# Optimization experiments

Measured on AMD Instinct MI355X. Metric: run time of the kernel, lower is better.

## Reference

```python
import jax, jax.numpy as jnp
import numpy as np

EPS = 1e-5  # torch InstanceNorm2d default eps

def conv1x1(x, w, b):
    # x: [B,C,H,W], w: [O,C], b: [O]
    return jnp.einsum('bchw,oc->bohw', x, w) + b[None, :, None, None]

def instance_norm(x):
    # InstanceNorm2d(affine=False): normalize per-sample, per-channel over H,W
    mean = jnp.mean(x, axis=(2, 3), keepdims=True)
    var = jnp.var(x, axis=(2, 3), keepdims=True)
    return (x - mean) * jax.lax.rsqrt(var + EPS)

def proj(x, w, b):
    return jax.nn.relu(instance_norm(conv1x1(x, w, b)))

def setup_inputs() -> dict:
    key = jax.random.key(0)
    ks = jax.random.split(key, 9)
    B, C, Ci, H, W = 16, 256, 128, 64, 64
    s_in = 1.0 / np.sqrt(C)
    s_mid = 1.0 / np.sqrt(Ci)
    return {
        'x': jax.random.normal(ks[0], (B, C, H, W), jnp.float32),
        'g_w': jax.random.normal(ks[1], (Ci, C), jnp.float32) * s_in,
        'g_b': jax.random.normal(ks[2], (Ci,), jnp.float32) * s_in,
        'theta_w': jax.random.normal(ks[3], (Ci, C), jnp.float32) * s_in,
        'theta_b': jax.random.normal(ks[4], (Ci,), jnp.float32) * s_in,
        'phi_w': jax.random.normal(ks[5], (Ci, C), jnp.float32) * s_in,
        'phi_b': jax.random.normal(ks[6], (Ci,), jnp.float32) * s_in,
        'W_w': jax.random.normal(ks[7], (C, Ci), jnp.float32) * s_mid,
        'W_b': jax.random.normal(ks[8], (C,), jnp.float32) * s_mid,
    }

def reference(x, g_w, g_b, theta_w, theta_b, phi_w, phi_b, W_w, W_b):
    B, C, H, W = x.shape
    Ci = g_w.shape[0]
    N = H * W
    g_x = proj(x, g_w, g_b).reshape(B, Ci, N)        # [B,Ci,N]
    theta_x = proj(x, theta_w, theta_b).reshape(B, Ci, N)
    phi_x = proj(x, phi_w, phi_b).reshape(B, Ci, N)
    # channel-attention Gram matrix [B,Ci,Ci], softmax over last dim
    f = jnp.einsum('bin,bjn->bij', theta_x, phi_x)
    attn = jax.nn.softmax(f, axis=2)
    y = jnp.einsum('bij,bjn->bin', attn, g_x)        # [B,Ci,N]
    # replicate torch permute(0,2,1).contiguous().view(B,Ci,H,W)
    y = jnp.transpose(y, (0, 2, 1)).reshape(B, Ci, H, W)
    y = instance_norm(conv1x1(y, W_w, W_b))
    return y + x
```

## Files before the change

kernel.cpp:

```cpp
#include <hip/hip_runtime.h>

#define DEVINL __device__ __forceinline__

typedef __attribute__((ext_vector_type(8))) short bf8v;
typedef __attribute__((ext_vector_type(4))) float f32x4;
typedef __attribute__((ext_vector_type(8))) unsigned short us8;
typedef __attribute__((ext_vector_type(4))) unsigned short us4;

DEVINL unsigned short f2bf(float f) {
  unsigned int u = __builtin_bit_cast(unsigned int, f);
  u += 0x7fffu + ((u >> 16) & 1u);
  return (unsigned short)(u >> 16);
}
DEVINL unsigned short f2bf_trunc(float f) {
  return (unsigned short)(__builtin_bit_cast(unsigned int, f) >> 16);
}
DEVINL float bf2f(unsigned short h) {
  unsigned int u = ((unsigned int)h) << 16;
  return __builtin_bit_cast(float, u);
}

__global__ __launch_bounds__(512, 4)
void proj_gemm(const unsigned short* __restrict__ wall_hi,
               const unsigned short* __restrict__ wall_lo,
               const float* __restrict__ x,
               unsigned short* __restrict__ zr_hi, unsigned short* __restrict__ zr_lo,
               float* __restrict__ partials)
{
  __shared__ __align__(16) unsigned short As_hi[384 * 40];
  __shared__ __align__(16) unsigned short As_lo[256 * 40];
  __shared__ __align__(16) unsigned short Bs_hi[64 * 40];
  __shared__ __align__(16) unsigned short Bs_lo[64 * 40];

  const int t = threadIdx.x;
  const int lane = t & 63;
  const int wave = t >> 6;
  const int wm = wave >> 1, wn = wave & 1;
  const int lr = lane & 15, lk = lane >> 4;
  const int b = blockIdx.z;
  const int bx = blockIdx.x;
  const int nbase = bx * 64;
  const float* xs = x + (long)b * 256 * 4096;

  f32x4 acc[6][2];
#pragma unroll
  for (int i = 0; i < 6; ++i)
#pragma unroll
    for (int j = 0; j < 2; ++j) acc[i][j] = (f32x4)0.0f;

  for (int kt = 0; kt < 8; ++kt) {
    const int k0 = kt * 32;
#pragma unroll
    for (int i = 0; i < 3; ++i) {
      const int q = i * 512 + t;
      const int row = q >> 2, c = q & 3;
      *(us8*)&As_hi[row * 40 + c * 8] = *(const us8*)&wall_hi[(long)row * 256 + k0 + c * 8];
    }
#pragma unroll
    for (int i = 0; i < 2; ++i) {
      const int q = i * 512 + t;
      const int row = q >> 2, c = q & 3;
      *(us8*)&As_lo[row * 40 + c * 8] = *(const us8*)&wall_lo[(long)row * 256 + k0 + c * 8];
    }
    const int nl = t & 63, cg = t >> 6;
    float xv[4];
#pragma unroll
    for (int i = 0; i < 4; ++i)
      xv[i] = xs[(long)(k0 + cg * 4 + i) * 4096 + nbase + nl];
    us4 h4, l4;
#pragma unroll
    for (int e = 0; e < 4; ++e) {
      const float v = xv[e];
      const unsigned short hb = f2bf(v);
      h4[e] = hb;
      l4[e] = f2bf_trunc(v - bf2f(hb));
    }
    *(us4*)&Bs_hi[nl * 40 + cg * 4] = h4;
    *(us4*)&Bs_lo[nl * 40 + cg * 4] = l4;
    __syncthreads();

    const int ko = lk * 8;
    bf8v bh[2], bl[2];
#pragma unroll
    for (int ni = 0; ni < 2; ++ni) {
      const int r = (wn * 32 + ni * 16 + lr) * 40 + ko;
      bh[ni] = *(const bf8v*)&Bs_hi[r];
      bl[ni] = *(const bf8v*)&Bs_lo[r];
    }
#pragma unroll
    for (int mi = 0; mi < 6; ++mi) {
      const int fr = mi * 4 + wm;
      const int r = (fr * 16 + lr) * 40 + ko;
      const bf8v ah = *(const bf8v*)&As_hi[r];
      if (fr < 16) {
        const bf8v al = *(const bf8v*)&As_lo[r];
#pragma unroll
        for (int ni = 0; ni < 2; ++ni) {
          acc[mi][ni] = __builtin_amdgcn_mfma_f32_16x16x32_bf16(bh[ni], ah, acc[mi][ni], 0, 0, 0);
          acc[mi][ni] = __builtin_amdgcn_mfma_f32_16x16x32_bf16(bl[ni], ah, acc[mi][ni], 0, 0, 0);
          acc[mi][ni] = __builtin_amdgcn_mfma_f32_16x16x32_bf16(bh[ni], al, acc[mi][ni], 0, 0, 0);
        }
      } else {
#pragma unroll
        for (int ni = 0; ni < 2; ++ni)
          acc[mi][ni] = __builtin_amdgcn_mfma_f32_16x16x32_bf16(bh[ni], ah, acc[mi][ni], 0, 0, 0);
      }
    }
    __syncthreads();
  }

  float* sbuf = (float*)As_hi;
#pragma unroll
  for (int mi = 0; mi < 6; ++mi) {
    float s = 0.f, ss = 0.f;
#pragma unroll
    for (int ni = 0; ni < 2; ++ni)
#pragma unroll
      for (int r = 0; r < 4; ++r) {
        const float v = acc[mi][ni][r];
        s += v; ss += v * v;
      }
    const int fr = mi * 4 + wm;
    const int slot = ((fr * 16 + lr) * 8 + (wn * 4 + lk)) * 2;
    sbuf[slot] = s; sbuf[slot + 1] = ss;
  }
  __syncthreads();
  if (t < 384) {
    float s = 0.f, ss = 0.f;
#pragma unroll
    for (int w = 0; w < 8; ++w) {
      s += sbuf[(t * 8 + w) * 2];
      ss += sbuf[(t * 8 + w) * 2 + 1];
    }
    const long pidx = ((long)bx * 6144 + b * 384 + t) * 2;
    partials[pidx] = s; partials[pidx + 1] = ss;
  }

#pragma unroll
  for (int mi = 0; mi < 6; ++mi)
#pragma unroll
    for (int ni = 0; ni < 2; ++ni) {
      const int gm = (mi * 4 + wm) * 16 + lr;
      const int gn = nbase + wn * 32 + ni * 16 + lk * 4;
      const long o = ((long)b * 384 + gm) * 4096 + gn;
      us4 hv, lv;
#pragma unroll
      for (int r = 0; r < 4; ++r) {
        const float v = acc[mi][ni][r];
        const unsigned short h = f2bf(v);
        hv[r] = h;
        lv[r] = f2bf_trunc(v - bf2f(h));
      }
      *(us4*)&zr_hi[o] = hv;
      *(us4*)&zr_lo[o] = lv;
    }
}

__global__ __launch_bounds__(256)
void stats_reduce(const float* __restrict__ partials, float* __restrict__ stats)
{
  const int row = blockIdx.x * 256 + threadIdx.x;
  float s = 0.f, ss = 0.f;
#pragma unroll
  for (int k = 0; k < 64; ++k) {
    s += partials[((long)k * 6144 + row) * 2];
    ss += partials[((long)k * 6144 + row) * 2 + 1];
  }
  const float mean = s * (1.f / 4096.f);
  const float var = ss * (1.f / 4096.f) - mean * mean;
  const float rs = rsqrtf(fmaxf(var, 0.f) + 1e-5f);
  stats[row * 2] = rs;
  stats[row * 2 + 1] = -mean * rs;
}

__global__ __launch_bounds__(256, 4)
void fgemm_norm(const unsigned short* __restrict__ zr_hi, const unsigned short* __restrict__ zr_lo,
                const float* __restrict__ stats, float* __restrict__ fpart)
{
  __shared__ __align__(16) unsigned short As_hi[128 * 72];
  __shared__ __align__(16) unsigned short As_lo[128 * 72];
  __shared__ __align__(16) unsigned short Bs_hi[128 * 72];
  __shared__ __align__(16) unsigned short Bs_lo[128 * 72];

  const int t = threadIdx.x;
  const int lane = t & 63;
  const int wave = t >> 6;
  const int wm = wave >> 1, wn = wave & 1;
  const int lr = lane & 15, lk = lane >> 4;
  const int zb = blockIdx.z >> 5, z1 = blockIdx.z & 31;
  const int koff = z1 * 128;

  f32x4 acc[4][4];
#pragma unroll
  for (int i = 0; i < 4; ++i)
#pragma unroll
    for (int j = 0; j < 4; ++j) acc[i][j] = (f32x4)0.0f;

  for (int kt = 0; kt < 2; ++kt) {
    const int k0 = koff + kt * 64;
#pragma unroll
    for (int i = 0; i < 4; ++i) {
      const int q = i * 256 + t;
      const int row = q >> 3, c = q & 7;
#pragma unroll
      for (int op = 0; op < 2; ++op) {
        const int grow = zb * 384 + op * 128 + row;
        const long g = (long)grow * 4096 + k0 + c * 8;
        const us8 h = *(const us8*)&zr_hi[g];
        const us8 l = *(const us8*)&zr_lo[g];
        const float rs = stats[grow * 2];
        const float nmrs = stats[grow * 2 + 1];
        us8 oh, ol;
#pragma unroll
        for (int e = 0; e < 8; ++e) {
          const float v = bf2f(h[e]) + bf2f(l[e]);
          const float nv = fmaxf(__builtin_fmaf(v, rs, nmrs), 0.f);
          const unsigned short hb = f2bf(nv);
          oh[e] = hb;
          ol[e] = f2bf_trunc(nv - bf2f(hb));
        }
        unsigned short* dh = op ? Bs_hi : As_hi;
        unsigned short* dl = op ? Bs_lo : As_lo;
        *(us8*)&dh[row * 72 + c * 8] = oh;
        *(us8*)&dl[row * 72 + c * 8] = ol;
      }
    }
    __syncthreads();
#pragma unroll
    for (int ks = 0; ks < 2; ++ks) {
      const int ko = ks * 32 + lk * 8;
      bf8v ah[4], bh[4], al[4], bl[4];
#pragma unroll
      for (int mi = 0; mi < 4; ++mi) {
        const int r = (wm * 64 + mi * 16 + lr) * 72 + ko;
        ah[mi] = *(const bf8v*)&As_hi[r];
        al[mi] = *(const bf8v*)&As_lo[r];
      }
#pragma unroll
      for (int ni = 0; ni < 4; ++ni) {
        const int r = (wn * 64 + ni * 16 + lr) * 72 + ko;
        bh[ni] = *(const bf8v*)&Bs_hi[r];
        bl[ni] = *(const bf8v*)&Bs_lo[r];
      }
#pragma unroll
      for (int mi = 0; mi < 4; ++mi)
#pragma unroll
        for (int ni = 0; ni < 4; ++ni) {
          acc[mi][ni] = __builtin_amdgcn_mfma_f32_16x16x32_bf16(bh[ni], ah[mi], acc[mi][ni], 0, 0, 0);
          acc[mi][ni] = __builtin_amdgcn_mfma_f32_16x16x32_bf16(bl[ni], ah[mi], acc[mi][ni], 0, 0, 0);
          acc[mi][ni] = __builtin_amdgcn_mfma_f32_16x16x32_bf16(bh[ni], al[mi], acc[mi][ni], 0, 0, 0);
        }
    }
    __syncthreads();
  }

  const long cOff = ((long)zb * 32 + z1) * 16384;
#pragma unroll
  for (int mi = 0; mi < 4; ++mi)
#pragma unroll
    for (int ni = 0; ni < 4; ++ni) {
      const int gm = wm * 64 + mi * 16 + lr;
      const int gn = wn * 64 + ni * 16 + lk * 4;
      *(f32x4*)&fpart[cOff + (long)gm * 128 + gn] = acc[mi][ni];
    }
}

template<bool OUT_BF16>
__global__ __launch_bounds__(256, 2)
void gemm_tn(const unsigned short* __restrict__ Ah0, const unsigned short* __restrict__ Bh0,
             void* __restrict__ Cout,
             int lda, int ldb, int ldc, int ksteps, int z1count,
             long aS1, long aS2, long bS1, long bS2, long cS1, long cS2)
{
  __shared__ __align__(16) unsigned short As_hi[128 * 72];
  __shared__ __align__(16) unsigned short Bs_hi[128 * 72];

  const int t = threadIdx.x;
  const int lane = t & 63;
  const int wave = t >> 6;
  const int wm = wave >> 1, wn = wave & 1;
  const int lr = lane & 15, lk = lane >> 4;

  const int z = blockIdx.z;
  const int zb = z / z1count, z1 = z - zb * z1count;
  const unsigned short* Ah = Ah0 + zb * aS2 + z1 * aS1;
  const unsigned short* Bh = Bh0 + zb * bS2 + z1 * bS1;
  const long cOff = zb * cS2 + z1 * cS1;

  const int mbase = blockIdx.y * 128;
  const int nbase = blockIdx.x * 128;

  f32x4 acc[4][4];
#pragma unroll
  for (int i = 0; i < 4; ++i)
#pragma unroll
    for (int j = 0; j < 4; ++j) acc[i][j] = (f32x4)0.0f;

  for (int kt = 0; kt < ksteps; ++kt) {
    const int k0 = kt * 64;
#pragma unroll
    for (int i = 0; i < 4; ++i) {
      const int q = i * 256 + t;
      const int row = q >> 3, c = q & 7;
      const int lo = row * 72 + c * 8;
      *(us8*)&As_hi[lo] = *(const us8*)&Ah[(long)(mbase + row) * lda + k0 + c * 8];
      *(us8*)&Bs_hi[lo] = *(const us8*)&Bh[(long)(nbase + row) * ldb + k0 + c * 8];
    }
    __syncthreads();
#pragma unroll
    for (int ks = 0; ks < 2; ++ks) {
      const int ko = ks * 32 + lk * 8;
      bf8v ah[4], bh[4];
#pragma unroll
      for (int mi = 0; mi < 4; ++mi)
        ah[mi] = *(const bf8v*)&As_hi[(wm * 64 + mi * 16 + lr) * 72 + ko];
#pragma unroll
      for (int ni = 0; ni < 4; ++ni)
        bh[ni] = *(const bf8v*)&Bs_hi[(wn * 64 + ni * 16 + lr) * 72 + ko];
#pragma unroll
      for (int mi = 0; mi < 4; ++mi)
#pragma unroll
        for (int ni = 0; ni < 4; ++ni)
          acc[mi][ni] = __builtin_amdgcn_mfma_f32_16x16x32_bf16(bh[ni], ah[mi], acc[mi][ni], 0, 0, 0);
    }
    __syncthreads();
  }

#pragma unroll
  for (int mi = 0; mi < 4; ++mi)
#pragma unroll
    for (int ni = 0; ni < 4; ++ni) {
      const int gm = mbase + wm * 64 + mi * 16 + lr;
      const int gn = nbase + wn * 64 + ni * 16 + lk * 4;
      const f32x4 v = acc[mi][ni];
      if (OUT_BF16) {
        us4 o;
#pragma unroll
        for (int r = 0; r < 4; ++r) o[r] = f2bf(v[r]);
        *(us4*)&((unsigned short*)Cout)[cOff + (long)gm * ldc + gn] = o;
      } else {
        *(f32x4*)&((float*)Cout)[cOff + (long)gm * ldc + gn] = v;
      }
    }
}

__global__ __launch_bounds__(256)
void prep_weights(const float* __restrict__ g_w, const float* __restrict__ th_w,
                  const float* __restrict__ ph_w, const float* __restrict__ W_w,
                  unsigned short* __restrict__ wall_hi, unsigned short* __restrict__ wall_lo,
                  unsigned short* __restrict__ w2h)
{
  const int i = blockIdx.x * 256 + threadIdx.x;
  float v;
  if (i < 32768) v = th_w[i];
  else if (i < 65536) v = ph_w[i - 32768];
  else v = g_w[i - 65536];
  const unsigned short h = f2bf(v);
  wall_hi[i] = h;
  if (i < 65536) wall_lo[i] = f2bf_trunc(v - bf2f(h));
  if (i < 32768) w2h[i] = f2bf(W_w[i]);
}

__global__ __launch_bounds__(256)
void norm_transpose_g(const unsigned short* __restrict__ zr_hi,
                      const unsigned short* __restrict__ zr_lo,
                      const float* __restrict__ stats,
                      unsigned short* __restrict__ gT)
{
  __shared__ unsigned short T[64 * 136];
  const int b = blockIdx.y, n0 = blockIdx.x * 64;
  const int t = threadIdx.x;
  const int c = t >> 1, part = t & 1;
  const int grow = b * 384 + 256 + c;
  const float rs = stats[grow * 2];
  const float nmrs = stats[grow * 2 + 1];
  const long off = (long)grow * 4096 + n0 + part * 32;
#pragma unroll
  for (int j = 0; j < 8; ++j) {
    const us4 h = *(const us4*)&zr_hi[off + j * 4];
    const us4 l = *(const us4*)&zr_lo[off + j * 4];
#pragma unroll
    for (int e = 0; e < 4; ++e) {
      const float v = bf2f(h[e]) + bf2f(l[e]);
      const float nv = fmaxf(__builtin_fmaf(v, rs, nmrs), 0.f);
      T[(part * 32 + j * 4 + e) * 136 + c] = f2bf(nv);
    }
  }
  __syncthreads();
  const int nl = t >> 2, q = t & 3;
  const long obase = ((long)b * 4096 + n0 + nl) * 128 + q * 32;
#pragma unroll
  for (int k = 0; k < 4; ++k) {
    us8 o;
#pragma unroll
    for (int e = 0; e < 8; ++e) o[e] = T[nl * 136 + q * 32 + k * 8 + e];
    *(us8*)&gT[obase + k * 8] = o;
  }
}

__global__ __launch_bounds__(64)
void softmax_attn(const float* __restrict__ fpart, unsigned short* __restrict__ attn)
{
  const int row = blockIdx.x;
  const int b = row >> 7, i = row & 127;
  const int t = threadIdx.x;
  float v0 = 0.f, v1 = 0.f;
#pragma unroll
  for (int kc = 0; kc < 32; ++kc) {
    const float* p = fpart + ((long)(b * 32 + kc)) * 16384 + i * 128;
    v0 += p[t];
    v1 += p[t + 64];
  }
  float mx = fmaxf(v0, v1);
  for (int o = 32; o > 0; o >>= 1) mx = fmaxf(mx, __shfl_xor(mx, o));
  const float e0 = __expf(v0 - mx), e1 = __expf(v1 - mx);
  float s = e0 + e1;
  for (int o = 32; o > 0; o >>= 1) s += __shfl_xor(s, o);
  const float inv = 1.f / s;
  attn[(long)row * 128 + t] = f2bf(e0 * inv);
  attn[(long)row * 128 + t + 64] = f2bf(e1 * inv);
}

__global__ __launch_bounds__(256)
void finalize(const unsigned short* __restrict__ z2b, const float* __restrict__ x,
              float* __restrict__ out)
{
  const int row = blockIdx.x;
  const long base = (long)row * 4096;
  const int t = threadIdx.x;
  float v[16];
  float s = 0.f, ss = 0.f;
#pragma unroll
  for (int h = 0; h < 2; ++h) {
    us8 u = *(const us8*)&z2b[base + t * 16 + h * 8];
#pragma unroll
    for (int e = 0; e < 8; ++e) {
      const float f = bf2f(u[e]);
      v[h * 8 + e] = f;
      s += f; ss += f * f;
    }
  }
  __shared__ float r0[256], r1[256];
  r0[t] = s; r1[t] = ss;
  __syncthreads();
  for (int o = 128; o > 0; o >>= 1) {
    if (t < o) { r0[t] += r0[t + o]; r1[t] += r1[t + o]; }
    __syncthreads();
  }
  const float mean = r0[0] * (1.f / 4096.f);
  const float var = r1[0] * (1.f / 4096.f) - mean * mean;
  const float rs = rsqrtf(fmaxf(var, 0.f) + 1e-5f);
#pragma unroll
  for (int i = 0; i < 4; ++i) {
    f32x4 xr = *(const f32x4*)&x[base + t * 16 + i * 4];
    f32x4 o;
#pragma unroll
    for (int e = 0; e < 4; ++e) o[e] = (v[i * 4 + e] - mean) * rs + xr[e];
    *(f32x4*)&out[base + t * 16 + i * 4] = o;
  }
}

extern "C" void kernel_launch(void* const* d_in, const int* in_sizes, int n_in,
                              void* d_out, int out_size, void* d_ws, size_t ws_size,
                              hipStream_t stream)
{
  const float* x    = (const float*)d_in[0];
  const float* g_w  = (const float*)d_in[1];
  const float* th_w = (const float*)d_in[3];
  const float* ph_w = (const float*)d_in[5];
  const float* W_w  = (const float*)d_in[7];

  char* ws = (char*)d_ws;
  const size_t MB = 1024ull * 1024ull;
  if (ws_size < 186 * MB) return;

  unsigned short* zr_hi    = (unsigned short*)(ws);
  unsigned short* zr_lo    = (unsigned short*)(ws + 48 * MB);
  float*          fpart    = (float*)(ws + 96 * MB);
  unsigned short* attn     = (unsigned short*)(ws + 128 * MB);
  unsigned short* gT       = (unsigned short*)(ws + 132 * MB);
  unsigned short* y4T      = (unsigned short*)(ws + 148 * MB);
  unsigned short* z2b      = (unsigned short*)(ws);
  float*          partials = (float*)(ws + 164 * MB);
  float*          stats    = (float*)(ws + 167 * MB);
  unsigned short* wall_hi  = (unsigned short*)(ws + 168 * MB);
  unsigned short* wall_lo  = (unsigned short*)(ws + 168 * MB + 256 * 1024);
  unsigned short* w2h      = (unsigned short*)(ws + 168 * MB + 512 * 1024);

  prep_weights<<<dim3(384), 256, 0, stream>>>(g_w, th_w, ph_w, W_w, wall_hi, wall_lo, w2h);

  proj_gemm<<<dim3(64, 1, 16), 512, 0, stream>>>(wall_hi, wall_lo, x, zr_hi, zr_lo, partials);

  stats_reduce<<<dim3(24), 256, 0, stream>>>(partials, stats);

  norm_transpose_g<<<dim3(64, 16), 256, 0, stream>>>(zr_hi, zr_lo, stats, gT);

  fgemm_norm<<<dim3(1, 1, 512), 256, 0, stream>>>(zr_hi, zr_lo, stats, fpart);

  softmax_attn<<<dim3(2048), 64, 0, stream>>>(fpart, attn);

  gemm_tn<true><<<dim3(1, 1, 512), 256, 0, stream>>>(
      attn, gT, y4T,
      128, 4096, 128, 2, 32,
      0, 16384, 128, (long)4096 * 128, 16384, (long)4096 * 128);

  gemm_tn<true><<<dim3(32, 2, 16), 256, 0, stream>>>(
      w2h, y4T, z2b,
      128, 128, 4096, 2, 1,
      0, 0, 0, (long)4096 * 128, 0, (long)256 * 4096);

  finalize<<<dim3(4096), 256, 0, stream>>>(z2b, x, (float*)d_out);
}
```

Before: 174.4 us.

## Enlarge proj GEMM tile with register prefetch, drop g lo-plane, specialise conv2 GEMM

The projection GEMM now uses 128-column N tiles with K=64 steps and loads the next x slice into registers while MFMAs run. This halves the block count and the per-block weight reloads. The g projection's low-precision correction plane is no longer written, and norm_transpose_g reads only the hi plane, which cuts memory traffic but slightly lowers precision for g. The conv2 GEMM becomes a dedicated kernel whose 256x128 tile covers all output channels, so each y4T tile is read only once. The larger shared-memory footprint and 96 accumulators lower occupancy, traded against fewer barriers and better reuse.

```diff
diff --git a/kernel.cpp b/kernel.cpp
--- a/kernel.cpp
+++ b/kernel.cpp
@@ -20,17 +20,17 @@
   return __builtin_bit_cast(float, u);
 }
 
-__global__ __launch_bounds__(512, 4)
+__global__ __launch_bounds__(512, 2)
 void proj_gemm(const unsigned short* __restrict__ wall_hi,
                const unsigned short* __restrict__ wall_lo,
                const float* __restrict__ x,
                unsigned short* __restrict__ zr_hi, unsigned short* __restrict__ zr_lo,
                float* __restrict__ partials)
 {
-  __shared__ __align__(16) unsigned short As_hi[384 * 40];
-  __shared__ __align__(16) unsigned short As_lo[256 * 40];
-  __shared__ __align__(16) unsigned short Bs_hi[64 * 40];
-  __shared__ __align__(16) unsigned short Bs_lo[64 * 40];
+  __shared__ __align__(16) unsigned short As_hi[384 * 72];
+  __shared__ __align__(16) unsigned short As_lo[256 * 72];
+  __shared__ __align__(16) unsigned short Bs_hi[128 * 72];
+  __shared__ __align__(16) unsigned short Bs_lo[128 * 72];
 
   const int t = threadIdx.x;
   const int lane = t & 63;
@@ -39,71 +39,86 @@
   const int lr = lane & 15, lk = lane >> 4;
   const int b = blockIdx.z;
   const int bx = blockIdx.x;
-  const int nbase = bx * 64;
+  const int nbase = bx * 128;
   const float* xs = x + (long)b * 256 * 4096;
 
-  f32x4 acc[6][2];
+  const int nl = t & 127, cg = t >> 7;
+  float xv[16];
+
+  f32x4 acc[6][4];
 #pragma unroll
   for (int i = 0; i < 6; ++i)
 #pragma unroll
-    for (int j = 0; j < 2; ++j) acc[i][j] = (f32x4)0.0f;
-
-  for (int kt = 0; kt < 8; ++kt) {
-    const int k0 = kt * 32;
-#pragma unroll
-    for (int i = 0; i < 3; ++i) {
+    for (int j = 0; j < 4; ++j) acc[i][j] = (f32x4)0.0f;
+
+#pragma unroll
+  for (int i = 0; i < 16; ++i)
+    xv[i] = xs[(long)(cg * 16 + i) * 4096 + nbase + nl];
+
+  for (int kt = 0; kt < 4; ++kt) {
+    const int k0 = kt * 64;
+#pragma unroll
+    for (int i = 0; i < 6; ++i) {
       const int q = i * 512 + t;
-      const int row = q >> 2, c = q & 3;
-      *(us8*)&As_hi[row * 40 + c * 8] = *(const us8*)&wall_hi[(long)row * 256 + k0 + c * 8];
-    }
-#pragma unroll
-    for (int i = 0; i < 2; ++i) {
+      const int row = q >> 3, c = q & 7;
+      *(us8*)&As_hi[row * 72 + c * 8] = *(const us8*)&wall_hi[(long)row * 256 + k0 + c * 8];
+    }
+#pragma unroll
+    for (int i = 0; i < 4; ++i) {
       const int q = i * 512 + t;
-      const int row = q >> 2, c = q & 3;
-      *(us8*)&As_lo[row * 40 + c * 8] = *(const us8*)&wall_lo[(long)row * 256 + k0 + c * 8];
-    }
-    const int nl = t & 63, cg = t >> 6;
-    float xv[4];
-#pragma unroll
-    for (int i = 0; i < 4; ++i)
-      xv[i] = xs[(long)(k0 + cg * 4 + i) * 4096 + nbase + nl];
-    us4 h4, l4;
-#pragma unroll
-    for (int e = 0; e < 4; ++e) {
-      const float v = xv[e];
-      const unsigned short hb = f2bf(v);
-      h4[e] = hb;
-      l4[e] = f2bf_trunc(v - bf2f(hb));
-    }
-    *(us4*)&Bs_hi[nl * 40 + cg * 4] = h4;
-    *(us4*)&Bs_lo[nl * 40 + cg * 4] = l4;
-    __syncthreads();
-
-    const int ko = lk * 8;
-    bf8v bh[2], bl[2];
-#pragma unroll
-    for (int ni = 0; ni < 2; ++ni) {
-      const int r = (wn * 32 + ni * 16 + lr) * 40 + ko;
-      bh[ni] = *(const bf8v*)&Bs_hi[r];
-      bl[ni] = *(const bf8v*)&Bs_lo[r];
-    }
-#pragma unroll
-    for (int mi = 0; mi < 6; ++mi) {
-      const int fr = mi * 4 + wm;
-      const int r = (fr * 16 + lr) * 40 + ko;
-      const bf8v ah = *(const bf8v*)&As_hi[r];
-      if (fr < 16) {
-        const bf8v al = *(const bf8v*)&As_lo[r];
-#pragma unroll
-        for (int ni = 0; ni < 2; ++ni) {
-          acc[mi][ni] = __builtin_amdgcn_mfma_f32_16x16x32_bf16(bh[ni], ah, acc[mi][ni], 0, 0, 0);
-          acc[mi][ni] = __builtin_amdgcn_mfma_f32_16x16x32_bf16(bl[ni], ah, acc[mi][ni], 0, 0, 0);
-          acc[mi][ni] = __builtin_amdgcn_mfma_f32_16x16x32_bf16(bh[ni], al, acc[mi][ni], 0, 0, 0);
+      const int row = q >> 3, c = q & 7;
+      *(us8*)&As_lo[row * 72 + c * 8] = *(const us8*)&wall_lo[(long)row * 256 + k0 + c * 8];
+    }
+#pragma unroll
+    for (int ch = 0; ch < 2; ++ch) {
+      us8 h8, l8;
+#pragma unroll
+      for (int e = 0; e < 8; ++e) {
+        const float v = xv[ch * 8 + e];
+        const unsigned short hb = f2bf(v);
+        h8[e] = hb;
+        l8[e] = f2bf_trunc(v - bf2f(hb));
+      }
+      *(us8*)&Bs_hi[nl * 72 + cg * 16 + ch * 8] = h8;
+      *(us8*)&Bs_lo[nl * 72 + cg * 16 + ch * 8] = l8;
+    }
+    __syncthreads();
+
+    if (kt < 3) {
+      const int kn = (kt + 1) * 64;
+#pragma unroll
+      for (int i = 0; i < 16; ++i)
+        xv[i] = xs[(long)(kn + cg * 16 + i) * 4096 + nbase + nl];
+    }
+
+#pragma unroll
+    for (int ks = 0; ks < 2; ++ks) {
+      const int ko = ks * 32 + lk * 8;
+      bf8v bh[4], bl[4];
+#pragma unroll
+      for (int ni = 0; ni < 4; ++ni) {
+        const int r = (wn * 64 + ni * 16 + lr) * 72 + ko;
+        bh[ni] = *(const bf8v*)&Bs_hi[r];
+        bl[ni] = *(const bf8v*)&Bs_lo[r];
+      }
+#pragma unroll
+      for (int mi = 0; mi < 6; ++mi) {
+        const int fr = mi * 4 + wm;
+        const int r = (fr * 16 + lr) * 72 + ko;
+        const bf8v ah = *(const bf8v*)&As_hi[r];
+        if (fr < 16) {
+          const bf8v al = *(const bf8v*)&As_lo[r];
+#pragma unroll
+          for (int ni = 0; ni < 4; ++ni) {
+            acc[mi][ni] = __builtin_amdgcn_mfma_f32_16x16x32_bf16(bh[ni], ah, acc[mi][ni], 0, 0, 0);
+            acc[mi][ni] = __builtin_amdgcn_mfma_f32_16x16x32_bf16(bl[ni], ah, acc[mi][ni], 0, 0, 0);
+            acc[mi][ni] = __builtin_amdgcn_mfma_f32_16x16x32_bf16(bh[ni], al, acc[mi][ni], 0, 0, 0);
+          }
+        } else {
+#pragma unroll
+          for (int ni = 0; ni < 4; ++ni)
+            acc[mi][ni] = __builtin_amdgcn_mfma_f32_16x16x32_bf16(bh[ni], ah, acc[mi][ni], 0, 0, 0);
         }
-      } else {
-#pragma unroll
-        for (int ni = 0; ni < 2; ++ni)
-          acc[mi][ni] = __builtin_amdgcn_mfma_f32_16x16x32_bf16(bh[ni], ah, acc[mi][ni], 0, 0, 0);
       }
     }
     __syncthreads();
@@ -114,7 +129,7 @@
   for (int mi = 0; mi < 6; ++mi) {
     float s = 0.f, ss = 0.f;
 #pragma unroll
-    for (int ni = 0; ni < 2; ++ni)
+    for (int ni = 0; ni < 4; ++ni)
 #pragma unroll
       for (int r = 0; r < 4; ++r) {
         const float v = acc[mi][ni][r];
@@ -139,9 +154,9 @@
 #pragma unroll
   for (int mi = 0; mi < 6; ++mi)
 #pragma unroll
-    for (int ni = 0; ni < 2; ++ni) {
+    for (int ni = 0; ni < 4; ++ni) {
       const int gm = (mi * 4 + wm) * 16 + lr;
-      const int gn = nbase + wn * 32 + ni * 16 + lk * 4;
+      const int gn = nbase + wn * 64 + ni * 16 + lk * 4;
       const long o = ((long)b * 384 + gm) * 4096 + gn;
       us4 hv, lv;
 #pragma unroll
@@ -152,7 +167,7 @@
         lv[r] = f2bf_trunc(v - bf2f(h));
       }
       *(us4*)&zr_hi[o] = hv;
-      *(us4*)&zr_lo[o] = lv;
+      if (gm < 256) *(us4*)&zr_lo[o] = lv;
     }
 }
 
@@ -162,7 +177,7 @@
   const int row = blockIdx.x * 256 + threadIdx.x;
   float s = 0.f, ss = 0.f;
 #pragma unroll
-  for (int k = 0; k < 64; ++k) {
+  for (int k = 0; k < 32; ++k) {
     s += partials[((long)k * 6144 + row) * 2];
     ss += partials[((long)k * 6144 + row) * 2 + 1];
   }
@@ -265,12 +280,11 @@
     }
 }
 
-template<bool OUT_BF16>
 __global__ __launch_bounds__(256, 2)
-void gemm_tn(const unsigned short* __restrict__ Ah0, const unsigned short* __restrict__ Bh0,
-             void* __restrict__ Cout,
-             int lda, int ldb, int ldc, int ksteps, int z1count,
-             long aS1, long aS2, long bS1, long bS2, long cS1, long cS2)
+void gemm_y(const unsigned short* __restrict__ Ah0, const unsigned short* __restrict__ Bh0,
+            unsigned short* __restrict__ Cout,
+            int lda, int ldb, int ldc, int ksteps, int z1count,
+            long aS1, long aS2, long bS1, long bS2, long cS1, long cS2)
 {
   __shared__ __align__(16) unsigned short As_hi[128 * 72];
   __shared__ __align__(16) unsigned short Bs_hi[128 * 72];
@@ -287,9 +301,6 @@
   const unsigned short* Bh = Bh0 + zb * bS2 + z1 * bS1;
   const long cOff = zb * cS2 + z1 * cS1;
 
-  const int mbase = blockIdx.y * 128;
-  const int nbase = blockIdx.x * 128;
-
   f32x4 acc[4][4];
 #pragma unroll
   for (int i = 0; i < 4; ++i)
@@ -303,8 +314,8 @@
       const int q = i * 256 + t;
       const int row = q >> 3, c = q & 7;
       const int lo = row * 72 + c * 8;
-      *(us8*)&As_hi[lo] = *(const us8*)&Ah[(long)(mbase + row) * lda + k0 + c * 8];
-      *(us8*)&Bs_hi[lo] = *(const us8*)&Bh[(long)(nbase + row) * ldb + k0 + c * 8];
+      *(us8*)&As_hi[lo] = *(const us8*)&Ah[(long)row * lda + k0 + c * 8];
+      *(us8*)&Bs_hi[lo] = *(const us8*)&Bh[(long)row * ldb + k0 + c * 8];
     }
     __syncthreads();
 #pragma unroll
@@ -330,17 +341,84 @@
   for (int mi = 0; mi < 4; ++mi)
 #pragma unroll
     for (int ni = 0; ni < 4; ++ni) {
-      const int gm = mbase + wm * 64 + mi * 16 + lr;
+      const int gm = wm * 64 + mi * 16 + lr;
+      const int gn = wn * 64 + ni * 16 + lk * 4;
+      const f32x4 v = acc[mi][ni];
+      us4 o;
+#pragma unroll
+      for (int r = 0; r < 4; ++r) o[r] = f2bf(v[r]);
+      *(us4*)&Cout[cOff + (long)gm * ldc + gn] = o;
+    }
+}
+
+__global__ __launch_bounds__(256, 2)
+void conv2_gemm(const unsigned short* __restrict__ w2h,
+                const unsigned short* __restrict__ y4T,
+                unsigned short* __restrict__ z2b)
+{
+  __shared__ __align__(16) unsigned short As_hi[256 * 72];
+  __shared__ __align__(16) unsigned short Bs_hi[128 * 72];
+
+  const int t = threadIdx.x;
+  const int lane = t & 63;
+  const int wave = t >> 6;
+  const int wm = wave >> 1, wn = wave & 1;
+  const int lr = lane & 15, lk = lane >> 4;
+  const int b = blockIdx.z;
+  const int nbase = blockIdx.x * 128;
+  const unsigned short* Bh = y4T + (long)b * 4096 * 128 + (long)nbase * 128;
+
+  f32x4 acc[8][4];
+#pragma unroll
+  for (int i = 0; i < 8; ++i)
+#pragma unroll
+    for (int j = 0; j < 4; ++j) acc[i][j] = (f32x4)0.0f;
+
+  for (int kt = 0; kt < 2; ++kt) {
+    const int k0 = kt * 64;
+#pragma unroll
+    for (int i = 0; i < 8; ++i) {
+      const int q = i * 256 + t;
+      const int row = q >> 3, c = q & 7;
+      *(us8*)&As_hi[row * 72 + c * 8] = *(const us8*)&w2h[(long)row * 128 + k0 + c * 8];
+    }
+#pragma unroll
+    for (int i = 0; i < 4; ++i) {
+      const int q = i * 256 + t;
+      const int row = q >> 3, c = q & 7;
+      *(us8*)&Bs_hi[row * 72 + c * 8] = *(const us8*)&Bh[(long)row * 128 + k0 + c * 8];
+    }
+    __syncthreads();
+#pragma unroll
+    for (int ks = 0; ks < 2; ++ks) {
+      const int ko = ks * 32 + lk * 8;
+      bf8v ah[8], bh[4];
+#pragma unroll
+      for (int mi = 0; mi < 8; ++mi)
+        ah[mi] = *(const bf8v*)&As_hi[(wm * 128 + mi * 16 + lr) * 72 + ko];
+#pragma unroll
+      for (int ni = 0; ni < 4; ++ni)
+        bh[ni] = *(const bf8v*)&Bs_hi[(wn * 64 + ni * 16 + lr) * 72 + ko];
+#pragma unroll
+      for (int mi = 0; mi < 8; ++mi)
+#pragma unroll
+        for (int ni = 0; ni < 4; ++ni)
+          acc[mi][ni] = __builtin_amdgcn_mfma_f32_16x16x32_bf16(bh[ni], ah[mi], acc[mi][ni], 0, 0, 0);
+    }
+    __syncthreads();
+  }
+
+#pragma unroll
+  for (int mi = 0; mi < 8; ++mi)
+#pragma unroll
+    for (int ni = 0; ni < 4; ++ni) {
+      const int gm = wm * 128 + mi * 16 + lr;
       const int gn = nbase + wn * 64 + ni * 16 + lk * 4;
       const f32x4 v = acc[mi][ni];
-      if (OUT_BF16) {
-        us4 o;
-#pragma unroll
-        for (int r = 0; r < 4; ++r) o[r] = f2bf(v[r]);
-        *(us4*)&((unsigned short*)Cout)[cOff + (long)gm * ldc + gn] = o;
-      } else {
-        *(f32x4*)&((float*)Cout)[cOff + (long)gm * ldc + gn] = v;
-      }
+      us4 o;
+#pragma unroll
+      for (int r = 0; r < 4; ++r) o[r] = f2bf(v[r]);
+      *(us4*)&z2b[((long)b * 256 + gm) * 4096 + gn] = o;
     }
 }
 
@@ -363,7 +441,6 @@
 
 __global__ __launch_bounds__(256)
 void norm_transpose_g(const unsigned short* __restrict__ zr_hi,
-                      const unsigned short* __restrict__ zr_lo,
                       const float* __restrict__ stats,
                       unsigned short* __restrict__ gT)
 {
@@ -376,14 +453,13 @@
   const float nmrs = stats[grow * 2 + 1];
   const long off = (long)grow * 4096 + n0 + part * 32;
 #pragma unroll
-  for (int j = 0; j < 8; ++j) {
-    const us4 h = *(const us4*)&zr_hi[off + j * 4];
-    const us4 l = *(const us4*)&zr_lo[off + j * 4];
-#pragma unroll
-    for (int e = 0; e < 4; ++e) {
-      const float v = bf2f(h[e]) + bf2f(l[e]);
+  for (int j = 0; j < 4; ++j) {
+    const us8 h = *(const us8*)&zr_hi[off + j * 8];
+#pragma unroll
+    for (int e = 0; e < 8; ++e) {
+      const float v = bf2f(h[e]);
       const float nv = fmaxf(__builtin_fmaf(v, rs, nmrs), 0.f);
-      T[(part * 32 + j * 4 + e) * 136 + c] = f2bf(nv);
+      T[(part * 32 + j * 8 + e) * 136 + c] = f2bf(nv);
     }
   }
   __syncthreads();
@@ -489,25 +565,22 @@
 
   prep_weights<<<dim3(384), 256, 0, stream>>>(g_w, th_w, ph_w, W_w, wall_hi, wall_lo, w2h);
 
-  proj_gemm<<<dim3(64, 1, 16), 512, 0, stream>>>(wall_hi, wall_lo, x, zr_hi, zr_lo, partials);
+  proj_gemm<<<dim3(32, 1, 16), 512, 0, stream>>>(wall_hi, wall_lo, x, zr_hi, zr_lo, partials);
 
   stats_reduce<<<dim3(24), 256, 0, stream>>>(partials, stats);
 
-  norm_transpose_g<<<dim3(64, 16), 256, 0, stream>>>(zr_hi, zr_lo, stats, gT);
+  norm_transpose_g<<<dim3(64, 16), 256, 0, stream>>>(zr_hi, stats, gT);
 
   fgemm_norm<<<dim3(1, 1, 512), 256, 0, stream>>>(zr_hi, zr_lo, stats, fpart);
 
   softmax_attn<<<dim3(2048), 64, 0, stream>>>(fpart, attn);
 
-  gemm_tn<true><<<dim3(1, 1, 512), 256, 0, stream>>>(
+  gemm_y<<<dim3(1, 1, 512), 256, 0, stream>>>(
       attn, gT, y4T,
       128, 4096, 128, 2, 32,
       0, 16384, 128, (long)4096 * 128, 16384, (long)4096 * 128);
 
-  gemm_tn<true><<<dim3(32, 2, 16), 256, 0, stream>>>(
-      w2h, y4T, z2b,
-      128, 128, 4096, 2, 1,
-      0, 0, 0, (long)4096 * 128, 0, (long)256 * 4096);
+  conv2_gemm<<<dim3(32, 1, 16), 256, 0, stream>>>(w2h, y4T, z2b);
 
   finalize<<<dim3(4096), 256, 0, stream>>>(z2b, x, (float*)d_out);
 }
```

Measured after the change: 160.8 us. -7.8%, faster.
